# Optimization experiments

Measured on AMD Instinct MI355X. Metric: run time of the kernel, lower is better.

## Reference

```python
import jax, jax.numpy as jnp
import numpy as np

TEMPERATURE = 0.07
COS_EPS = 1e-8  # torch F.cosine_similarity clamps norms at eps=1e-8


def setup_inputs() -> dict:
    key = jax.random.key(0)
    features = jax.random.normal(key, (8192, 1024), dtype=jnp.float32)
    return {"features": features}


def reference(features):
    n = features.shape[0]
    b = n // 2
    # Cosine similarity as normalize + GEMM (equivalent to broadcasted F.cosine_similarity)
    norms = jnp.maximum(jnp.linalg.norm(features, axis=1, keepdims=True), COS_EPS)
    fn = features / norms                      # [N, D]
    sim = (fn @ fn.T) / TEMPERATURE            # [N, N]
    # Mask self-similarity on the diagonal with -inf
    diag = jnp.eye(n, dtype=bool)
    sim = jnp.where(diag, -jnp.inf, sim)
    # labels: positive of i is its paired augmentation (i+b mod n)
    labels = jnp.concatenate([jnp.arange(b) + b, jnp.arange(b)])  # [N]
    # Cross-entropy in one stable pass
    log_probs = jax.nn.log_softmax(sim, axis=1)
    loss = -jnp.mean(log_probs[jnp.arange(n), labels])
    return loss
```

## Files before the change

### kernel.cpp

```cpp
#include <hip/hip_runtime.h>
#include <hip/hip_bf16.h>

#define N_ROWS 8192
#define D_DIM  1024
#define HALF_N 4096
#define N_TILES 2080
#define N_RED  8
constexpr float INV_T = 1.0f / 0.07f;

typedef __attribute__((ext_vector_type(4))) float f32x4;
typedef __attribute__((ext_vector_type(2))) long long2_;

__device__ __forceinline__ void async_ld16(const void* g, void* lds) {
    __builtin_amdgcn_global_load_lds(
        (const __attribute__((address_space(1))) void*)g,
        (__attribute__((address_space(3))) void*)lds,
        16, 0, 0);
}

__device__ __forceinline__ unsigned int pk_fp8x4(float a, float b, float c, float d) {
    int v = __builtin_amdgcn_cvt_pk_fp8_f32(a, b, 0, false);
    v = __builtin_amdgcn_cvt_pk_fp8_f32(c, d, v, true);
    return (unsigned int)v;
}

__global__ __launch_bounds__(256) void norm_kernel(const float* __restrict__ feat,
                                                   unsigned char* __restrict__ fn8,
                                                   float* __restrict__ row_sum,
                                                   unsigned int* __restrict__ done_cnt,
                                                   unsigned int* __restrict__ fin_cnt,
                                                   float* __restrict__ loss_acc) {
    const int w = threadIdx.x >> 6, lane = threadIdx.x & 63;
    const int row = blockIdx.x * 4 + w;
    if (blockIdx.x == 0 && threadIdx.x == 0) {
        *done_cnt = 0u;
        *fin_cnt = 0u;
        *loss_acc = 0.f;
    }
    const float4* src = (const float4*)(feat + (size_t)row * D_DIM);
    float4 v[4];
    float ss = 0.f;
#pragma unroll
    for (int t = 0; t < 4; ++t) {
        v[t] = src[lane + 64 * t];
        ss += v[t].x * v[t].x + v[t].y * v[t].y + v[t].z * v[t].z + v[t].w * v[t].w;
    }
#pragma unroll
    for (int off = 32; off; off >>= 1) ss += __shfl_xor(ss, off);
    float nrm = fmaxf(sqrtf(ss), 1e-8f);
    if (lane == 0) row_sum[row] = 0.f;
    const float inv = 1.0f / nrm;
    unsigned int* dst = (unsigned int*)(fn8 + (size_t)row * D_DIM);
#pragma unroll
    for (int t = 0; t < 4; ++t)
        dst[lane + 64 * t] = pk_fp8x4(v[t].x * inv, v[t].y * inv, v[t].z * inv, v[t].w * inv);
}

__global__ __launch_bounds__(256) void simgemm_kernel(const unsigned char* __restrict__ fn8,
                                                      float* __restrict__ row_sum,
                                                      float* __restrict__ s_target,
                                                      unsigned int* __restrict__ done_cnt,
                                                      unsigned int* __restrict__ fin_cnt,
                                                      float* __restrict__ loss_acc,
                                                      float* __restrict__ out) {
    __shared__ __align__(16) unsigned char As[128 * 64];
    __shared__ __align__(16) unsigned char Bs[128 * 64];
    const int t = blockIdx.x;
    int a = (int)((sqrtf(8.f * (float)t + 1.f) - 1.f) * 0.5f);
    while ((a + 1) * (a + 2) / 2 <= t) ++a;
    while (a * (a + 1) / 2 > t) --a;
    const int I = t - a * (a + 1) / 2;
    const int J = a;
    const int r0 = I * 128, c0 = J * 128;
    const bool isdiag = (I == J);
    const bool haspair = (J == I + 32);

    const int tid = threadIdx.x;
    const int w = tid >> 6, lane = tid & 63;
    const int q = lane >> 4, c16 = lane & 15;
    const int wr = (w >> 1) * 64;
    const int wc = (w & 1) * 64;
    const int wr4 = (w >> 1) * 4;
    const int wc4 = (w & 1) * 4;
    const int srow = lane >> 2;
    const int skoff = ((lane & 3) ^ ((srow >> 1) & 3)) * 16;
    const int lfo = c16 * 64 + ((q ^ ((c16 >> 1) & 3)) * 16);

    const unsigned char* pa0 = fn8 + (size_t)(r0 + w * 32 + srow) * D_DIM + skoff;
    const unsigned char* pa1 = pa0 + 16 * D_DIM;
    const unsigned char* pb0 = fn8 + (size_t)(c0 + w * 32 + srow) * D_DIM + skoff;
    const unsigned char* pb1 = pb0 + 16 * D_DIM;

    f32x4 acc[4][4];
#pragma unroll
    for (int i = 0; i < 4; ++i)
#pragma unroll
        for (int j = 0; j < 4; ++j) acc[i][j] = (f32x4){0.f, 0.f, 0.f, 0.f};

    for (int kt = 0; kt < 16; ++kt) {
        __syncthreads();
        async_ld16(pa0, (void*)&As[(w * 2 + 0) * 1024]);
        async_ld16(pa1, (void*)&As[(w * 2 + 1) * 1024]);
        async_ld16(pb0, (void*)&Bs[(w * 2 + 0) * 1024]);
        async_ld16(pb1, (void*)&Bs[(w * 2 + 1) * 1024]);
        pa0 += 64; pa1 += 64; pb0 += 64; pb1 += 64;
        __syncthreads();

        long2_ af[4], bf[4];
#pragma unroll
        for (int i = 0; i < 4; ++i)
            af[i] = *(const long2_*)&As[(wr4 + i) * 1024 + lfo];
#pragma unroll
        for (int j = 0; j < 4; ++j)
            bf[j] = *(const long2_*)&Bs[(wc4 + j) * 1024 + lfo];
#pragma unroll
        for (int i = 0; i < 4; ++i)
#pragma unroll
            for (int j = 0; j < 4; ++j) {
                acc[i][j] = __builtin_amdgcn_mfma_f32_16x16x32_fp8_fp8(
                    af[i].x, bf[j].x, acc[i][j], 0, 0, 0);
                acc[i][j] = __builtin_amdgcn_mfma_f32_16x16x32_fp8_fp8(
                    af[i].y, bf[j].y, acc[i][j], 0, 0, 0);
            }
    }

    float cs[4] = {0.f, 0.f, 0.f, 0.f};
#pragma unroll
    for (int i = 0; i < 4; ++i) {
        const int growb = r0 + wr + i * 16 + q * 4;
#pragma unroll
        for (int r = 0; r < 4; ++r) {
            const int grow = growb + r;
            float s = 0.f;
#pragma unroll
            for (int j = 0; j < 4; ++j) {
                const int gcol = c0 + wc + j * 16 + c16;
                float sim = acc[i][j][r] * INV_T;
                float e = __expf(sim - INV_T);
                if (isdiag && grow == gcol) e = 0.f;
                if (haspair && gcol == grow + HALF_N) {
                    __hip_atomic_store(&s_target[grow], sim, __ATOMIC_RELAXED,
                                       __HIP_MEMORY_SCOPE_AGENT);
                    __hip_atomic_store(&s_target[gcol], sim, __ATOMIC_RELAXED,
                                       __HIP_MEMORY_SCOPE_AGENT);
                }
                s += e;
                cs[j] += e;
            }
            s += __shfl_xor(s, 1);
            s += __shfl_xor(s, 2);
            s += __shfl_xor(s, 4);
            s += __shfl_xor(s, 8);
            if (c16 == 0) atomicAdd(&row_sum[grow], s);
        }
    }
    if (!isdiag) {
#pragma unroll
        for (int j = 0; j < 4; ++j) {
            float s = cs[j];
            s += __shfl_xor(s, 16);
            s += __shfl_xor(s, 32);
            if (q == 0) atomicAdd(&row_sum[c0 + wc + j * 16 + c16], s);
        }
    }

    __syncthreads();
    __shared__ unsigned int my_ord;
    if (tid == 0)
        my_ord = __hip_atomic_fetch_add(done_cnt, 1u, __ATOMIC_RELAXED,
                                        __HIP_MEMORY_SCOPE_AGENT);
    __syncthreads();
    const unsigned int ord = my_ord;
    if (ord >= N_TILES - N_RED) {
        if (tid == 0) {
            while (__hip_atomic_load(done_cnt, __ATOMIC_RELAXED,
                                     __HIP_MEMORY_SCOPE_AGENT) < N_TILES)
                __builtin_amdgcn_s_sleep(1);
        }
        __syncthreads();
        const int slice = (int)(ord - (N_TILES - N_RED));
        const int base_row = slice * (N_ROWS / N_RED) + tid * 4;
        float rv[4], sv[4];
#pragma unroll
        for (int u = 0; u < 4; ++u) {
            rv[u] = __hip_atomic_load(&row_sum[base_row + u], __ATOMIC_RELAXED,
                                      __HIP_MEMORY_SCOPE_AGENT);
            sv[u] = __hip_atomic_load(&s_target[base_row + u], __ATOMIC_RELAXED,
                                      __HIP_MEMORY_SCOPE_AGENT);
        }
        float local = 0.f;
#pragma unroll
        for (int u = 0; u < 4; ++u)
            local += __logf(rv[u]) - sv[u];
#pragma unroll
        for (int off = 32; off; off >>= 1) local += __shfl_xor(local, off);
        __shared__ float part[4];
        if ((tid & 63) == 0) part[tid >> 6] = local;
        __syncthreads();
        if (tid == 0) {
            float bsum = part[0] + part[1] + part[2] + part[3];
            __hip_atomic_fetch_add(loss_acc, bsum, __ATOMIC_RELAXED,
                                   __HIP_MEMORY_SCOPE_AGENT);
            unsigned int f = __hip_atomic_fetch_add(fin_cnt, 1u, __ATOMIC_ACQ_REL,
                                                    __HIP_MEMORY_SCOPE_AGENT);
            if (f == N_RED - 1) {
                float accv = __hip_atomic_load(loss_acc, __ATOMIC_RELAXED,
                                               __HIP_MEMORY_SCOPE_AGENT);
                out[0] = INV_T + accv * (1.0f / N_ROWS);
            }
        }
    }
}

extern "C" void kernel_launch(void* const* d_in, const int* in_sizes, int n_in,
                              void* d_out, int out_size, void* d_ws, size_t ws_size,
                              hipStream_t stream) {
    const float* feat = (const float*)d_in[0];
    float* out = (float*)d_out;
    char* ws = (char*)d_ws;

    unsigned char* fn8 = (unsigned char*)ws;
    size_t off = (size_t)N_ROWS * D_DIM;
    float* row_sum = (float*)(ws + off);   off += N_ROWS * sizeof(float);
    float* s_target = (float*)(ws + off);  off += N_ROWS * sizeof(float);
    unsigned int* done_cnt = (unsigned int*)(ws + off);  off += sizeof(unsigned int);
    unsigned int* fin_cnt = (unsigned int*)(ws + off);   off += sizeof(unsigned int);
    float* loss_acc = (float*)(ws + off);

    norm_kernel<<<N_ROWS / 4, 256, 0, stream>>>(feat, fn8, row_sum, done_cnt, fin_cnt, loss_acc);
    simgemm_kernel<<<N_TILES, 256, 0, stream>>>(fn8, row_sum, s_target, done_cnt, fin_cnt, loss_acc, out);
}
```

Baseline: 142.7 us.

## Convert similarity GEMM to persistent blocks with atomic tile queue

Launches a fixed grid of 1024 persistent workgroups that pull triangular tile indices from a global atomic counter instead of one workgroup per tile. The aim is to cut per-block launch and ramp-up overhead and to balance the tail, where the last finishers spin-wait and run the loss reduction. It adds an atomic fetch and two barriers per tile, and the spin-wait reducers now depend on other persistent blocks making progress.

```diff
diff --git a/kernel.cpp b/kernel.cpp
--- a/kernel.cpp
+++ b/kernel.cpp
@@ -6,6 +6,7 @@
 #define HALF_N 4096
 #define N_TILES 2080
 #define N_RED  8
+#define N_PERS 1024
 constexpr float INV_T = 1.0f / 0.07f;
 
 typedef __attribute__((ext_vector_type(4))) float f32x4;
@@ -29,13 +30,15 @@
                                                    float* __restrict__ row_sum,
                                                    unsigned int* __restrict__ done_cnt,
                                                    unsigned int* __restrict__ fin_cnt,
-                                                   float* __restrict__ loss_acc) {
+                                                   float* __restrict__ loss_acc,
+                                                   unsigned int* __restrict__ tile_cnt) {
     const int w = threadIdx.x >> 6, lane = threadIdx.x & 63;
     const int row = blockIdx.x * 4 + w;
     if (blockIdx.x == 0 && threadIdx.x == 0) {
         *done_cnt = 0u;
         *fin_cnt = 0u;
         *loss_acc = 0.f;
+        *tile_cnt = 0u;
     }
     const float4* src = (const float4*)(feat + (size_t)row * D_DIM);
     float4 v[4];
@@ -62,18 +65,11 @@
                                                       unsigned int* __restrict__ done_cnt,
                                                       unsigned int* __restrict__ fin_cnt,
                                                       float* __restrict__ loss_acc,
+                                                      unsigned int* __restrict__ tile_cnt,
                                                       float* __restrict__ out) {
     __shared__ __align__(16) unsigned char As[128 * 64];
     __shared__ __align__(16) unsigned char Bs[128 * 64];
-    const int t = blockIdx.x;
-    int a = (int)((sqrtf(8.f * (float)t + 1.f) - 1.f) * 0.5f);
-    while ((a + 1) * (a + 2) / 2 <= t) ++a;
-    while (a * (a + 1) / 2 > t) --a;
-    const int I = t - a * (a + 1) / 2;
-    const int J = a;
-    const int r0 = I * 128, c0 = J * 128;
-    const bool isdiag = (I == J);
-    const bool haspair = (J == I + 32);
+    __shared__ unsigned int my_ord, next_t;
 
     const int tid = threadIdx.x;
     const int w = tid >> 6, lane = tid & 63;
@@ -86,128 +82,149 @@
     const int skoff = ((lane & 3) ^ ((srow >> 1) & 3)) * 16;
     const int lfo = c16 * 64 + ((q ^ ((c16 >> 1) & 3)) * 16);
 
-    const unsigned char* pa0 = fn8 + (size_t)(r0 + w * 32 + srow) * D_DIM + skoff;
-    const unsigned char* pa1 = pa0 + 16 * D_DIM;
-    const unsigned char* pb0 = fn8 + (size_t)(c0 + w * 32 + srow) * D_DIM + skoff;
-    const unsigned char* pb1 = pb0 + 16 * D_DIM;
-
-    f32x4 acc[4][4];
-#pragma unroll
-    for (int i = 0; i < 4; ++i)
-#pragma unroll
-        for (int j = 0; j < 4; ++j) acc[i][j] = (f32x4){0.f, 0.f, 0.f, 0.f};
-
-    for (int kt = 0; kt < 16; ++kt) {
-        __syncthreads();
-        async_ld16(pa0, (void*)&As[(w * 2 + 0) * 1024]);
-        async_ld16(pa1, (void*)&As[(w * 2 + 1) * 1024]);
-        async_ld16(pb0, (void*)&Bs[(w * 2 + 0) * 1024]);
-        async_ld16(pb1, (void*)&Bs[(w * 2 + 1) * 1024]);
-        pa0 += 64; pa1 += 64; pb0 += 64; pb1 += 64;
-        __syncthreads();
-
-        long2_ af[4], bf[4];
-#pragma unroll
-        for (int i = 0; i < 4; ++i)
-            af[i] = *(const long2_*)&As[(wr4 + i) * 1024 + lfo];
-#pragma unroll
-        for (int j = 0; j < 4; ++j)
-            bf[j] = *(const long2_*)&Bs[(wc4 + j) * 1024 + lfo];
-#pragma unroll
-        for (int i = 0; i < 4; ++i)
-#pragma unroll
-            for (int j = 0; j < 4; ++j) {
-                acc[i][j] = __builtin_amdgcn_mfma_f32_16x16x32_fp8_fp8(
-                    af[i].x, bf[j].x, acc[i][j], 0, 0, 0);
-                acc[i][j] = __builtin_amdgcn_mfma_f32_16x16x32_fp8_fp8(
-                    af[i].y, bf[j].y, acc[i][j], 0, 0, 0);
-            }
-    }
-
-    float cs[4] = {0.f, 0.f, 0.f, 0.f};
-#pragma unroll
-    for (int i = 0; i < 4; ++i) {
-        const int growb = r0 + wr + i * 16 + q * 4;
-#pragma unroll
-        for (int r = 0; r < 4; ++r) {
-            const int grow = growb + r;
-            float s = 0.f;
-#pragma unroll
-            for (int j = 0; j < 4; ++j) {
-                const int gcol = c0 + wc + j * 16 + c16;
-                float sim = acc[i][j][r] * INV_T;
-                float e = __expf(sim - INV_T);
-                if (isdiag && grow == gcol) e = 0.f;
-                if (haspair && gcol == grow + HALF_N) {
-                    __hip_atomic_store(&s_target[grow], sim, __ATOMIC_RELAXED,
-                                       __HIP_MEMORY_SCOPE_AGENT);
-                    __hip_atomic_store(&s_target[gcol], sim, __ATOMIC_RELAXED,
-                                       __HIP_MEMORY_SCOPE_AGENT);
-                }
-                s += e;
-                cs[j] += e;
-            }
-            s += __shfl_xor(s, 1);
-            s += __shfl_xor(s, 2);
-            s += __shfl_xor(s, 4);
-            s += __shfl_xor(s, 8);
-            if (c16 == 0) atomicAdd(&row_sum[grow], s);
-        }
-    }
-    if (!isdiag) {
-#pragma unroll
-        for (int j = 0; j < 4; ++j) {
-            float s = cs[j];
-            s += __shfl_xor(s, 16);
-            s += __shfl_xor(s, 32);
-            if (q == 0) atomicAdd(&row_sum[c0 + wc + j * 16 + c16], s);
-        }
-    }
-
-    __syncthreads();
-    __shared__ unsigned int my_ord;
     if (tid == 0)
-        my_ord = __hip_atomic_fetch_add(done_cnt, 1u, __ATOMIC_RELAXED,
+        next_t = __hip_atomic_fetch_add(tile_cnt, 1u, __ATOMIC_RELAXED,
                                         __HIP_MEMORY_SCOPE_AGENT);
     __syncthreads();
-    const unsigned int ord = my_ord;
-    if (ord >= N_TILES - N_RED) {
-        if (tid == 0) {
-            while (__hip_atomic_load(done_cnt, __ATOMIC_RELAXED,
-                                     __HIP_MEMORY_SCOPE_AGENT) < N_TILES)
-                __builtin_amdgcn_s_sleep(1);
-        }
-        __syncthreads();
-        const int slice = (int)(ord - (N_TILES - N_RED));
-        const int base_row = slice * (N_ROWS / N_RED) + tid * 4;
-        float rv[4], sv[4];
-#pragma unroll
-        for (int u = 0; u < 4; ++u) {
-            rv[u] = __hip_atomic_load(&row_sum[base_row + u], __ATOMIC_RELAXED,
-                                      __HIP_MEMORY_SCOPE_AGENT);
-            sv[u] = __hip_atomic_load(&s_target[base_row + u], __ATOMIC_RELAXED,
-                                      __HIP_MEMORY_SCOPE_AGENT);
-        }
-        float local = 0.f;
-#pragma unroll
-        for (int u = 0; u < 4; ++u)
-            local += __logf(rv[u]) - sv[u];
-#pragma unroll
-        for (int off = 32; off; off >>= 1) local += __shfl_xor(local, off);
-        __shared__ float part[4];
-        if ((tid & 63) == 0) part[tid >> 6] = local;
+
+    while (true) {
+        const int t = (int)next_t;
+        if (t >= N_TILES) break;
+        int a = (int)((sqrtf(8.f * (float)t + 1.f) - 1.f) * 0.5f);
+        while ((a + 1) * (a + 2) / 2 <= t) ++a;
+        while (a * (a + 1) / 2 > t) --a;
+        const int I = t - a * (a + 1) / 2;
+        const int J = a;
+        const int r0 = I * 128, c0 = J * 128;
+        const bool isdiag = (I == J);
+        const bool haspair = (J == I + 32);
+
+        const unsigned char* pa0 = fn8 + (size_t)(r0 + w * 32 + srow) * D_DIM + skoff;
+        const unsigned char* pa1 = pa0 + 16 * D_DIM;
+        const unsigned char* pb0 = fn8 + (size_t)(c0 + w * 32 + srow) * D_DIM + skoff;
+        const unsigned char* pb1 = pb0 + 16 * D_DIM;
+
+        f32x4 acc[4][4];
+#pragma unroll
+        for (int i = 0; i < 4; ++i)
+#pragma unroll
+            for (int j = 0; j < 4; ++j) acc[i][j] = (f32x4){0.f, 0.f, 0.f, 0.f};
+
+        for (int kt = 0; kt < 16; ++kt) {
+            __syncthreads();
+            async_ld16(pa0, (void*)&As[(w * 2 + 0) * 1024]);
+            async_ld16(pa1, (void*)&As[(w * 2 + 1) * 1024]);
+            async_ld16(pb0, (void*)&Bs[(w * 2 + 0) * 1024]);
+            async_ld16(pb1, (void*)&Bs[(w * 2 + 1) * 1024]);
+            pa0 += 64; pa1 += 64; pb0 += 64; pb1 += 64;
+            __syncthreads();
+
+            long2_ af[4], bf[4];
+#pragma unroll
+            for (int i = 0; i < 4; ++i)
+                af[i] = *(const long2_*)&As[(wr4 + i) * 1024 + lfo];
+#pragma unroll
+            for (int j = 0; j < 4; ++j)
+                bf[j] = *(const long2_*)&Bs[(wc4 + j) * 1024 + lfo];
+#pragma unroll
+            for (int i = 0; i < 4; ++i)
+#pragma unroll
+                for (int j = 0; j < 4; ++j) {
+                    acc[i][j] = __builtin_amdgcn_mfma_f32_16x16x32_fp8_fp8(
+                        af[i].x, bf[j].x, acc[i][j], 0, 0, 0);
+                    acc[i][j] = __builtin_amdgcn_mfma_f32_16x16x32_fp8_fp8(
+                        af[i].y, bf[j].y, acc[i][j], 0, 0, 0);
+                }
+        }
+
+        float cs[4] = {0.f, 0.f, 0.f, 0.f};
+#pragma unroll
+        for (int i = 0; i < 4; ++i) {
+            const int growb = r0 + wr + i * 16 + q * 4;
+#pragma unroll
+            for (int r = 0; r < 4; ++r) {
+                const int grow = growb + r;
+                float s = 0.f;
+#pragma unroll
+                for (int j = 0; j < 4; ++j) {
+                    const int gcol = c0 + wc + j * 16 + c16;
+                    float sim = acc[i][j][r] * INV_T;
+                    float e = __expf(sim - INV_T);
+                    if (isdiag && grow == gcol) e = 0.f;
+                    if (haspair && gcol == grow + HALF_N) {
+                        __hip_atomic_store(&s_target[grow], sim, __ATOMIC_RELAXED,
+                                           __HIP_MEMORY_SCOPE_AGENT);
+                        __hip_atomic_store(&s_target[gcol], sim, __ATOMIC_RELAXED,
+                                           __HIP_MEMORY_SCOPE_AGENT);
+                    }
+                    s += e;
+                    cs[j] += e;
+                }
+                s += __shfl_xor(s, 1);
+                s += __shfl_xor(s, 2);
+                s += __shfl_xor(s, 4);
+                s += __shfl_xor(s, 8);
+                if (c16 == 0) atomicAdd(&row_sum[grow], s);
+            }
+        }
+        if (!isdiag) {
+#pragma unroll
+            for (int j = 0; j < 4; ++j) {
+                float s = cs[j];
+                s += __shfl_xor(s, 16);
+                s += __shfl_xor(s, 32);
+                if (q == 0) atomicAdd(&row_sum[c0 + wc + j * 16 + c16], s);
+            }
+        }
+
         __syncthreads();
         if (tid == 0) {
-            float bsum = part[0] + part[1] + part[2] + part[3];
-            __hip_atomic_fetch_add(loss_acc, bsum, __ATOMIC_RELAXED,
-                                   __HIP_MEMORY_SCOPE_AGENT);
-            unsigned int f = __hip_atomic_fetch_add(fin_cnt, 1u, __ATOMIC_ACQ_REL,
-                                                    __HIP_MEMORY_SCOPE_AGENT);
-            if (f == N_RED - 1) {
-                float accv = __hip_atomic_load(loss_acc, __ATOMIC_RELAXED,
-                                               __HIP_MEMORY_SCOPE_AGENT);
-                out[0] = INV_T + accv * (1.0f / N_ROWS);
-            }
+            my_ord = __hip_atomic_fetch_add(done_cnt, 1u, __ATOMIC_RELAXED,
+                                            __HIP_MEMORY_SCOPE_AGENT);
+            next_t = __hip_atomic_fetch_add(tile_cnt, 1u, __ATOMIC_RELAXED,
+                                            __HIP_MEMORY_SCOPE_AGENT);
+        }
+        __syncthreads();
+        const unsigned int ord = my_ord;
+        if (ord >= N_TILES - N_RED) {
+            if (tid == 0) {
+                while (__hip_atomic_load(done_cnt, __ATOMIC_RELAXED,
+                                         __HIP_MEMORY_SCOPE_AGENT) < N_TILES)
+                    __builtin_amdgcn_s_sleep(1);
+            }
+            __syncthreads();
+            const int slice = (int)(ord - (N_TILES - N_RED));
+            const int base_row = slice * (N_ROWS / N_RED) + tid * 4;
+            float rv[4], sv[4];
+#pragma unroll
+            for (int u = 0; u < 4; ++u) {
+                rv[u] = __hip_atomic_load(&row_sum[base_row + u], __ATOMIC_RELAXED,
+                                          __HIP_MEMORY_SCOPE_AGENT);
+                sv[u] = __hip_atomic_load(&s_target[base_row + u], __ATOMIC_RELAXED,
+                                          __HIP_MEMORY_SCOPE_AGENT);
+            }
+            float local = 0.f;
+#pragma unroll
+            for (int u = 0; u < 4; ++u)
+                local += __logf(rv[u]) - sv[u];
+#pragma unroll
+            for (int off = 32; off; off >>= 1) local += __shfl_xor(local, off);
+            __shared__ float part[4];
+            if ((tid & 63) == 0) part[tid >> 6] = local;
+            __syncthreads();
+            if (tid == 0) {
+                float bsum = part[0] + part[1] + part[2] + part[3];
+                __hip_atomic_fetch_add(loss_acc, bsum, __ATOMIC_RELAXED,
+                                       __HIP_MEMORY_SCOPE_AGENT);
+                unsigned int f = __hip_atomic_fetch_add(fin_cnt, 1u, __ATOMIC_ACQ_REL,
+                                                        __HIP_MEMORY_SCOPE_AGENT);
+                if (f == N_RED - 1) {
+                    float accv = __hip_atomic_load(loss_acc, __ATOMIC_RELAXED,
+                                                   __HIP_MEMORY_SCOPE_AGENT);
+                    out[0] = INV_T + accv * (1.0f / N_ROWS);
+                }
+            }
+            __syncthreads();
         }
     }
 }
@@ -225,8 +242,11 @@
     float* s_target = (float*)(ws + off);  off += N_ROWS * sizeof(float);
     unsigned int* done_cnt = (unsigned int*)(ws + off);  off += sizeof(unsigned int);
     unsigned int* fin_cnt = (unsigned int*)(ws + off);   off += sizeof(unsigned int);
-    float* loss_acc = (float*)(ws + off);
-
-    norm_kernel<<<N_ROWS / 4, 256, 0, stream>>>(feat, fn8, row_sum, done_cnt, fin_cnt, loss_acc);
-    simgemm_kernel<<<N_TILES, 256, 0, stream>>>(fn8, row_sum, s_target, done_cnt, fin_cnt, loss_acc, out);
-}
+    float* loss_acc = (float*)(ws + off);  off += sizeof(float);
+    unsigned int* tile_cnt = (unsigned int*)(ws + off);
+
+    norm_kernel<<<N_ROWS / 4, 256, 0, stream>>>(feat, fn8, row_sum, done_cnt, fin_cnt,
+                                                loss_acc, tile_cnt);
+    simgemm_kernel<<<N_PERS, 256, 0, stream>>>(fn8, row_sum, s_target, done_cnt, fin_cnt,
+                                               loss_acc, tile_cnt, out);
+}
```

New measurement: 170.7 us. +19.6%, slower.
